# Optimization experiments

Hardware: AMD Instinct MI355X
Metric: run time of the kernel (lower is better)

Reference implementation:

```python
import math
import jax, jax.numpy as jnp
import numpy as np

B, LD, LE = 8, 512, 512
D, H, DK, F, L, V = 1024, 16, 64, 4096, 3, 32000
EPS = 1e-5
NEG = -1000000000.0


def setup_inputs() -> dict:
    key = jax.random.key(0)
    ks = jax.random.split(key, 16)
    s = 0.02
    dec_inputs = jax.random.randint(ks[0], (B, LD), 0, V)
    # causal mask: True = masked out (matches masked_fill semantics)
    self_mask = jnp.broadcast_to(jnp.triu(jnp.ones((LD, LD), bool), k=1), (B, LD, LD))
    enc_output = jax.random.normal(ks[1], (B, LE, D), jnp.float32)
    encoder_mask = jnp.zeros((B, LD, LE), bool)  # no encoder padding
    embed = jax.random.normal(ks[2], (V, D), jnp.float32) * s
    # sinusoidal positional encoding, pe[:LD]
    pos = jnp.arange(LD, dtype=jnp.float32)[:, None]
    div = jnp.exp(jnp.arange(0, D, 2, dtype=jnp.float32) * (-math.log(10000.0) / D))
    pe = jnp.zeros((LD, D), jnp.float32)
    pe = pe.at[:, 0::2].set(jnp.sin(pos * div)).at[:, 1::2].set(jnp.cos(pos * div))
    # per-layer params; axis 1 of attn params: 0=self-attn, 1=enc-dec attn
    wq = jax.random.normal(ks[3], (L, 2, D, D), jnp.float32) * s
    wk = jax.random.normal(ks[4], (L, 2, D, D), jnp.float32) * s
    wv = jax.random.normal(ks[5], (L, 2, D, D), jnp.float32) * s
    wo = jax.random.normal(ks[6], (L, 2, D, D), jnp.float32) * s
    bq = jnp.zeros((L, 2, D), jnp.float32)
    bk = jnp.zeros((L, 2, D), jnp.float32)
    bv = jnp.zeros((L, 2, D), jnp.float32)
    bo = jnp.zeros((L, 2, D), jnp.float32)
    ffn_w1 = jax.random.normal(ks[7], (L, F, D), jnp.float32) * s
    ffn_b1 = jnp.zeros((L, F), jnp.float32)
    ffn_w2 = jax.random.normal(ks[8], (L, D, F), jnp.float32) * s
    ffn_b2 = jnp.zeros((L, D), jnp.float32)
    ln_g = jnp.ones((L, 3, D), jnp.float32)   # norm1/2/3 gains
    ln_b = jnp.zeros((L, 3, D), jnp.float32)  # norm1/2/3 biases
    return dict(dec_inputs=dec_inputs, self_mask=self_mask, enc_output=enc_output,
                encoder_mask=encoder_mask, embed=embed, pe=pe,
                wq=wq, bq=bq, wk=wk, bk=bk, wv=wv, bv=bv, wo=wo, bo=bo,
                ffn_w1=ffn_w1, ffn_b1=ffn_b1, ffn_w2=ffn_w2, ffn_b2=ffn_b2,
                ln_g=ln_g, ln_b=ln_b)


def _ln(x, g, b):
    m = jnp.mean(x, axis=-1, keepdims=True)
    v = jnp.mean((x - m) ** 2, axis=-1, keepdims=True)
    return (x - m) * jax.lax.rsqrt(v + EPS) * g + b


def _mha(qi, ki, vi, mask, wq, bq, wk, bk, wv, bv, wo, bo):
    Bq, Lq, _ = qi.shape
    Lk = ki.shape[1]
    Q = (qi @ wq.T + bq).reshape(Bq, Lq, H, DK).transpose(0, 2, 1, 3)
    K = (ki @ wk.T + bk).reshape(Bq, Lk, H, DK).transpose(0, 2, 1, 3)
    Vv = (vi @ wv.T + bv).reshape(Bq, Lk, H, DK).transpose(0, 2, 1, 3)
    scores = jnp.einsum('bhqd,bhkd->bhqk', Q, K) / math.sqrt(DK)
    scores = jnp.where(mask[:, None, :, :], NEG, scores)
    attn = jax.nn.softmax(scores, axis=-1)
    ctx = jnp.einsum('bhqk,bhkd->bhqd', attn, Vv)
    ctx = ctx.transpose(0, 2, 1, 3).reshape(Bq, Lq, H * DK)
    return ctx @ wo.T + bo


def reference(dec_inputs, self_mask, enc_output, encoder_mask, embed, pe,
              wq, bq, wk, bk, wv, bv, wo, bo,
              ffn_w1, ffn_b1, ffn_w2, ffn_b2, ln_g, ln_b):
    x = embed[dec_inputs] * math.sqrt(D) + pe[None, :, :]
    for l in range(L):
        h = _ln(x, ln_g[l, 0], ln_b[l, 0])
        a = _mha(h, h, h, self_mask,
                 wq[l, 0], bq[l, 0], wk[l, 0], bk[l, 0], wv[l, 0], bv[l, 0], wo[l, 0], bo[l, 0])
        x = x + a
        h = _ln(x, ln_g[l, 1], ln_b[l, 1])
        c = _mha(h, enc_output, enc_output, encoder_mask,
                 wq[l, 1], bq[l, 1], wk[l, 1], bk[l, 1], wv[l, 1], bv[l, 1], wo[l, 1], bo[l, 1])
        x = x + c
        h = _ln(x, ln_g[l, 2], ln_b[l, 2])
        f = jax.nn.relu(h @ ffn_w1[l].T + ffn_b1[l]) @ ffn_w2[l].T + ffn_b2[l]
        # faithful quirk of the source: residual is the cross-attn output, not x
        x = c + f
    return x
```

## Files before the change

### kernel.cpp

```cpp
#include <hip/hip_runtime.h>
#include <hip/hip_bf16.h>

using bf16x8 = __attribute__((ext_vector_type(8))) short;
using f32x4  = __attribute__((ext_vector_type(4))) float;
using u16x4  = __attribute__((ext_vector_type(4))) unsigned short;

#define DEVI static __device__ __forceinline__

DEVI unsigned short f2b(float f) {
  unsigned int u = __float_as_uint(f);
  u += 0x7FFFu + ((u >> 16) & 1u);
  return (unsigned short)(u >> 16);
}

DEVI void gload16(const unsigned short* g, unsigned short* l) {
  __builtin_amdgcn_global_load_lds(
      (const __attribute__((address_space(1))) unsigned int*)g,
      (__attribute__((address_space(3))) unsigned int*)l, 16, 0, 0);
}

DEVI float wred_max16(float v) {
#pragma unroll
  for (int m = 1; m < 16; m <<= 1) v = fmaxf(v, __shfl_xor(v, m, 64));
  return v;
}
DEVI float wred_sum16(float v) {
#pragma unroll
  for (int m = 1; m < 16; m <<= 1) v += __shfl_xor(v, m, 64);
  return v;
}


__global__ void cvt_kernel(const float* __restrict__ in,
                           unsigned short* __restrict__ out, int n4) {
  int i = blockIdx.x * blockDim.x + threadIdx.x;
  const int stride = gridDim.x * blockDim.x;
  for (; i < n4; i += stride) {
    const float4 v = ((const float4*)in)[i];
    u16x4 o;
    o[0] = f2b(v.x); o[1] = f2b(v.y); o[2] = f2b(v.z); o[3] = f2b(v.w);
    ((u16x4*)out)[i] = o;
  }
}

__global__ void pack_w(const float* __restrict__ s0,
                       const float* __restrict__ s1,
                       const float* __restrict__ s2,
                       int sub, unsigned short* __restrict__ dst, int nm) {
  const int r = blockIdx.x;
  const int m = blockIdx.y;
  const int l = blockIdx.z;
  const float* src = (m == 0 ? s0 : m == 1 ? s1 : s2)
                   + (size_t)(l * 2 + sub) * 1048576 + (size_t)r * 1024;
  unsigned short* d = dst + ((size_t)(l * nm + m) * 1024 + r) * 1024;
  const int col = threadIdx.x * 4;
  const float4 v = *(const float4*)(src + col);
  u16x4 o;
  o[0] = f2b(v.x); o[1] = f2b(v.y); o[2] = f2b(v.z); o[3] = f2b(v.w);
  *(u16x4*)(d + col) = o;
}

__global__ void pack_bias(const float* __restrict__ s0,
                          const float* __restrict__ s1,
                          const float* __restrict__ s2,
                          int sub, float* __restrict__ dst, int nm) {
  const int m = blockIdx.x, l = blockIdx.y;
  const float* src = (m == 0 ? s0 : m == 1 ? s1 : s2) + (size_t)(l * 2 + sub) * 1024;
  float* d = dst + ((size_t)l * nm + m) * 1024;
  const int i = threadIdx.x * 4;
  *(float4*)(d + i) = *(const float4*)(src + i);
}

__global__ void embed_kernel(const int* __restrict__ ids,
                             const float* __restrict__ emb,
                             const float* __restrict__ pe,
                             float* __restrict__ x) {
  const int row = blockIdx.x;
  const int t = row & 511;
  const int col = threadIdx.x * 4;
  const int id = ids[row];
  const float4 e = *(const float4*)(emb + (size_t)id * 1024 + col);
  const float4 p = *(const float4*)(pe + (size_t)t * 1024 + col);
  float4 o;
  o.x = e.x * 32.f + p.x; o.y = e.y * 32.f + p.y;
  o.z = e.z * 32.f + p.z; o.w = e.w * 32.f + p.w;
  *(float4*)(x + (size_t)row * 1024 + col) = o;
}

__global__ void ln_kernel(const float* __restrict__ x,
                          const float* __restrict__ g,
                          const float* __restrict__ b,
                          unsigned short* __restrict__ out) {
  const int row = blockIdx.x;
  const int l = threadIdx.x;
  const float4* xr = (const float4*)(x + (size_t)row * 1024);
  float4 v[4];
  float s = 0.f;
#pragma unroll
  for (int i = 0; i < 4; ++i) {
    v[i] = xr[l * 4 + i];
    s += v[i].x + v[i].y + v[i].z + v[i].w;
  }
#pragma unroll
  for (int m = 1; m < 64; m <<= 1) s += __shfl_xor(s, m, 64);
  const float mean = s * (1.f / 1024.f);
  float vs = 0.f;
#pragma unroll
  for (int i = 0; i < 4; ++i) {
    float dx = v[i].x - mean, dy = v[i].y - mean, dz = v[i].z - mean, dw = v[i].w - mean;
    vs += dx * dx + dy * dy + dz * dz + dw * dw;
  }
#pragma unroll
  for (int m = 1; m < 64; m <<= 1) vs += __shfl_xor(vs, m, 64);
  const float inv = rsqrtf(vs * (1.f / 1024.f) + 1e-5f);
#pragma unroll
  for (int i = 0; i < 4; ++i) {
    const int col = l * 16 + i * 4;
    const float4 gg = *(const float4*)(g + col);
    const float4 bb = *(const float4*)(b + col);
    u16x4 o;
    o[0] = f2b((v[i].x - mean) * inv * gg.x + bb.x);
    o[1] = f2b((v[i].y - mean) * inv * gg.y + bb.y);
    o[2] = f2b((v[i].z - mean) * inv * gg.z + bb.z);
    o[3] = f2b((v[i].w - mean) * inv * gg.w + bb.w);
    *(u16x4*)(out + (size_t)row * 1024 + col) = o;
  }
}

__global__ void vt_kernel(const unsigned short* __restrict__ Vsrc, int vsd,
                          unsigned short* __restrict__ Vt) {
  __shared__ alignas(16) unsigned short t[64][72];
  const int tt = blockIdx.x;
  const int h  = blockIdx.y;
  const int b  = blockIdx.z;
  const int tid = threadIdx.x;
  const int r  = tid >> 2;
  const int ch = tid & 3;
  const unsigned short* src =
      Vsrc + (size_t)(b * 512 + tt * 64 + r) * vsd + (size_t)h * 64 + ch * 16;
  const bf16x8 v0 = *(const bf16x8*)src;
  const bf16x8 v1 = *(const bf16x8*)(src + 8);
#pragma unroll
  for (int j = 0; j < 8; ++j) {
    t[ch * 16 + j][r]     = (unsigned short)v0[j];
    t[ch * 16 + 8 + j][r] = (unsigned short)v1[j];
  }
  __syncthreads();
  const int d  = tid >> 2;
  const int tp = tid & 3;
  unsigned short* dst = Vt + (((size_t)(b * 16 + h) * 64 + d) * 512) + tt * 64 + tp * 16;
  *(bf16x8*)dst       = *(const bf16x8*)&t[d][tp * 16];
  *(bf16x8*)(dst + 8) = *(const bf16x8*)&t[d][tp * 16 + 8];
}


enum { EPI_BF16 = 0, EPI_RELU_BF16 = 1, EPI_RES = 2, EPI_RES2 = 3 };

template<int EPI, int BM, int BN>
__global__ void gemm_bt(const unsigned short* __restrict__ A,
                        const unsigned short* __restrict__ Bw,
                        const float* __restrict__ bias,
                        int N, int K, int nn,
                        void* out0, const float* res, float* out1) {
  constexpr int MI = BM / 32;
  constexpr int NJ = BN / 32;
  __shared__ alignas(16) unsigned short As[2][BM * 64];
  __shared__ alignas(16) unsigned short Bs[2][BN * 64];
  const int tid = threadIdx.x;
  const int lane = tid & 63;
  const int wave = tid >> 6;
  int id = blockIdx.x;
  const int nwg = gridDim.x;
  id = (id & 7) * (nwg >> 3) + (id >> 3);
  const int bx = id % nn;
  const int by = id / nn;
  const int m0 = by * BM;
  const int n0 = bx * BN;
  const int wm = (wave >> 1) * (BM / 2);
  const int wn = (wave & 1) * (BN / 2);

  auto stage = [&](int buf, int kt) {
    const size_t k0 = (size_t)kt * 64;
#pragma unroll
    for (int i = 0; i < MI; ++i) {
      const int c = tid + 256 * i;
      const int row = c >> 3;
      const int lc = (c & 7) ^ (row & 7);
      gload16(A + (size_t)(m0 + row) * K + k0 + lc * 8, &As[buf][c * 8]);
    }
#pragma unroll
    for (int i = 0; i < NJ; ++i) {
      const int c = tid + 256 * i;
      const int row = c >> 3;
      const int lc = (c & 7) ^ (row & 7);
      gload16(Bw + (size_t)(n0 + row) * K + k0 + lc * 8, &Bs[buf][c * 8]);
    }
  };

  f32x4 acc[MI][NJ];
#pragma unroll
  for (int i = 0; i < MI; ++i)
#pragma unroll
    for (int j = 0; j < NJ; ++j) acc[i][j] = f32x4{0.f, 0.f, 0.f, 0.f};

  const int nk = K >> 6;
  stage(0, 0);
  int cur = 0;
  const int ro = lane & 15;
  const int hi = lane >> 4;
  for (int kt = 0; kt < nk; ++kt) {
    __syncthreads();
    if (kt + 1 < nk) stage(cur ^ 1, kt + 1);
    bf16x8 af[MI][2], bf[NJ][2];
#pragma unroll
    for (int i = 0; i < MI; ++i) {
      const int r = wm + i * 16 + ro;
#pragma unroll
      for (int ks = 0; ks < 2; ++ks)
        af[i][ks] = *(const bf16x8*)&As[cur][r * 64 + (((ks << 2) + hi) ^ (r & 7)) * 8];
    }
#pragma unroll
    for (int j = 0; j < NJ; ++j) {
      const int r = wn + j * 16 + ro;
#pragma unroll
      for (int ks = 0; ks < 2; ++ks)
        bf[j][ks] = *(const bf16x8*)&Bs[cur][r * 64 + (((ks << 2) + hi) ^ (r & 7)) * 8];
    }
#pragma unroll
    for (int ks = 0; ks < 2; ++ks)
#pragma unroll
      for (int i = 0; i < MI; ++i)
#pragma unroll
        for (int j = 0; j < NJ; ++j)
          acc[i][j] = __builtin_amdgcn_mfma_f32_16x16x32_bf16(af[i][ks], bf[j][ks], acc[i][j], 0, 0, 0);
    cur ^= 1;
  }

  const int r4 = hi * 4;
#pragma unroll
  for (int i = 0; i < MI; ++i) {
#pragma unroll
    for (int j = 0; j < NJ; ++j) {
      const int cg = n0 + wn + j * 16 + ro;
      const float bv = bias[cg];
#pragma unroll
      for (int q = 0; q < 4; ++q) {
        const int rg = m0 + wm + i * 16 + r4 + q;
        const size_t idx = (size_t)rg * N + cg;
        const float v = acc[i][j][q] + bv;
        if (EPI == EPI_BF16) {
          ((unsigned short*)out0)[idx] = f2b(v);
        } else if (EPI == EPI_RELU_BF16) {
          ((unsigned short*)out0)[idx] = f2b(fmaxf(v, 0.f));
        } else if (EPI == EPI_RES) {
          ((float*)out0)[idx] = res[idx] + v;
        } else {
          const float r = res[idx];
          ((float*)out0)[idx] = v;
          out1[idx] = r + v;
        }
      }
    }
  }
}


template<bool CAUSAL>
__global__ __launch_bounds__(64) void attn_kernel(
    const unsigned short* __restrict__ Qg, int qs,
    const unsigned short* __restrict__ Kg, int ksd,
    const unsigned short* __restrict__ Vt,
    unsigned short* __restrict__ Og) {
  __shared__ alignas(16) unsigned short Pl[32 * 64];
  const int qt = blockIdx.x;
  const int h  = blockIdx.y;
  const int b  = blockIdx.z;
  const int lane = threadIdx.x;
  const int ro = lane & 15;
  const int hi = lane >> 4;
  const size_t qbase = (size_t)b * 512 * qs  + (size_t)h * 64;
  const size_t kbase = (size_t)b * 512 * ksd + (size_t)h * 64;
  const size_t vbase = ((size_t)(b * 16 + h)) * 64 * 512;
  const size_t obase = (size_t)b * 512 * 1024 + (size_t)h * 64;

  bf16x8 qf[2][2];
#pragma unroll
  for (int mi = 0; mi < 2; ++mi)
#pragma unroll
    for (int ks = 0; ks < 2; ++ks)
      qf[mi][ks] = *(const bf16x8*)&Qg[qbase + (size_t)(qt * 32 + mi * 16 + ro) * qs + ks * 32 + hi * 8];

  f32x4 o[2][4];
  float mrun[2][4], lrun[2][4];
#pragma unroll
  for (int mi = 0; mi < 2; ++mi) {
#pragma unroll
    for (int di = 0; di < 4; ++di) o[mi][di] = f32x4{0.f, 0.f, 0.f, 0.f};
#pragma unroll
    for (int q = 0; q < 4; ++q) { mrun[mi][q] = -1e30f; lrun[mi][q] = 0.f; }
  }

  const int ktmax = CAUSAL ? (qt >> 1) : 7;
  for (int kt = 0; kt <= ktmax; ++kt) {
    bf16x8 kf[4][2];
#pragma unroll
    for (int ni = 0; ni < 4; ++ni)
#pragma unroll
      for (int ks = 0; ks < 2; ++ks)
        kf[ni][ks] = *(const bf16x8*)&Kg[kbase + (size_t)(kt * 64 + ni * 16 + ro) * ksd + ks * 32 + hi * 8];

    f32x4 s[2][4];
#pragma unroll
    for (int mi = 0; mi < 2; ++mi)
#pragma unroll
      for (int ni = 0; ni < 4; ++ni) s[mi][ni] = f32x4{0.f, 0.f, 0.f, 0.f};
#pragma unroll
    for (int ks = 0; ks < 2; ++ks)
#pragma unroll
      for (int mi = 0; mi < 2; ++mi)
#pragma unroll
        for (int ni = 0; ni < 4; ++ni)
          s[mi][ni] = __builtin_amdgcn_mfma_f32_16x16x32_bf16(qf[mi][ks], kf[ni][ks], s[mi][ni], 0, 0, 0);

#pragma unroll
    for (int mi = 0; mi < 2; ++mi)
#pragma unroll
      for (int ni = 0; ni < 4; ++ni)
#pragma unroll
        for (int q = 0; q < 4; ++q) {
          float e = s[mi][ni][q] * 0.125f;
          if (CAUSAL && kt == ktmax &&
              (kt * 64 + ni * 16 + ro) > (qt * 32 + mi * 16 + hi * 4 + q)) e = -1e9f;
          s[mi][ni][q] = e;
        }

    float fac[2][4];
#pragma unroll
    for (int mi = 0; mi < 2; ++mi)
#pragma unroll
      for (int q = 0; q < 4; ++q) {
        float rm = s[mi][0][q];
#pragma unroll
        for (int ni = 1; ni < 4; ++ni) rm = fmaxf(rm, s[mi][ni][q]);
        rm = wred_max16(rm);
        const float mn = fmaxf(mrun[mi][q], rm);
        fac[mi][q] = __expf(mrun[mi][q] - mn);
        mrun[mi][q] = mn;
      }
#pragma unroll
    for (int mi = 0; mi < 2; ++mi)
#pragma unroll
      for (int q = 0; q < 4; ++q) {
        float rs = 0.f;
#pragma unroll
        for (int ni = 0; ni < 4; ++ni) {
          const float pv = __expf(s[mi][ni][q] - mrun[mi][q]);
          s[mi][ni][q] = pv;
          rs += pv;
        }
        rs = wred_sum16(rs);
        lrun[mi][q] = lrun[mi][q] * fac[mi][q] + rs;
      }
#pragma unroll
    for (int mi = 0; mi < 2; ++mi)
#pragma unroll
      for (int di = 0; di < 4; ++di)
#pragma unroll
        for (int q = 0; q < 4; ++q) o[mi][di][q] *= fac[mi][q];

#pragma unroll
    for (int mi = 0; mi < 2; ++mi)
#pragma unroll
      for (int ni = 0; ni < 4; ++ni)
#pragma unroll
        for (int q = 0; q < 4; ++q) {
          const int row = mi * 16 + hi * 4 + q;
          const int col = ni * 16 + ro;
          const int sc  = ((col >> 3) ^ (row & 7)) * 8 + (col & 7);
          Pl[row * 64 + sc] = f2b(s[mi][ni][q]);
        }

    bf16x8 pa[2][2];
#pragma unroll
    for (int mi = 0; mi < 2; ++mi)
#pragma unroll
      for (int ks = 0; ks < 2; ++ks) {
        const int row = mi * 16 + ro;
        pa[mi][ks] = *(const bf16x8*)&Pl[row * 64 + (((ks << 2) + hi) ^ (row & 7)) * 8];
      }

#pragma unroll
    for (int di = 0; di < 4; ++di)
#pragma unroll
      for (int ks = 0; ks < 2; ++ks) {
        const bf16x8 vf = *(const bf16x8*)&Vt[vbase + (size_t)(di * 16 + ro) * 512 + kt * 64 + ks * 32 + hi * 8];
#pragma unroll
        for (int mi = 0; mi < 2; ++mi)
          o[mi][di] = __builtin_amdgcn_mfma_f32_16x16x32_bf16(pa[mi][ks], vf, o[mi][di], 0, 0, 0);
      }
  }

#pragma unroll
  for (int mi = 0; mi < 2; ++mi)
#pragma unroll
    for (int di = 0; di < 4; ++di)
#pragma unroll
      for (int q = 0; q < 4; ++q) {
        const float val = o[mi][di][q] / lrun[mi][q];
        Og[obase + (size_t)(qt * 32 + mi * 16 + hi * 4 + q) * 1024 + di * 16 + ro] = f2b(val);
      }
}


extern "C" void kernel_launch(void* const* d_in, const int* in_sizes, int n_in,
                              void* d_out, int out_size, void* d_ws, size_t ws_size,
                              hipStream_t stream) {
  (void)in_sizes; (void)n_in; (void)out_size; (void)ws_size;
  const int*   dec = (const int*)d_in[0];
  const float* enc = (const float*)d_in[2];
  const float* emb = (const float*)d_in[4];
  const float* pe  = (const float*)d_in[5];
  const float* wq  = (const float*)d_in[6];
  const float* bq  = (const float*)d_in[7];
  const float* wk  = (const float*)d_in[8];
  const float* bk  = (const float*)d_in[9];
  const float* wv  = (const float*)d_in[10];
  const float* bv  = (const float*)d_in[11];
  const float* wo  = (const float*)d_in[12];
  const float* bo  = (const float*)d_in[13];
  const float* w1  = (const float*)d_in[14];
  const float* b1  = (const float*)d_in[15];
  const float* w2  = (const float*)d_in[16];
  const float* b2  = (const float*)d_in[17];
  const float* lng = (const float*)d_in[18];
  const float* lnb = (const float*)d_in[19];

  const size_t SZ_ACT = 4194304ull;

  char* p = (char*)d_ws;
  auto alloc = [&](size_t bytes) { char* r = p; p += (bytes + 255) & ~(size_t)255; return r; };
  unsigned short* qkvw  = (unsigned short*)alloc(3ull * 3 * 1048576 * 2);
  unsigned short* kvw   = (unsigned short*)alloc(3ull * 2 * 1048576 * 2);
  unsigned short* wqxb  = (unsigned short*)alloc(3ull * 1048576 * 2);
  unsigned short* Wob   = (unsigned short*)alloc(6291456ull * 2);
  unsigned short* W1b   = (unsigned short*)alloc(12582912ull * 2);
  unsigned short* W2b   = (unsigned short*)alloc(12582912ull * 2);
  unsigned short* encb  = (unsigned short*)alloc(SZ_ACT * 2);
  float*          x     = (float*)alloc(SZ_ACT * 4);
  float*          c     = (float*)alloc(SZ_ACT * 4);
  unsigned short* hb    = (unsigned short*)alloc(SZ_ACT * 2);
  unsigned short* qkvb  = (unsigned short*)alloc(4096ull * 3072 * 2);
  unsigned short* kvb   = (unsigned short*)alloc(4096ull * 2048 * 2);
  unsigned short* qb    = (unsigned short*)alloc(SZ_ACT * 2);
  unsigned short* vtb   = (unsigned short*)alloc(SZ_ACT * 2);
  unsigned short* mid   = (unsigned short*)alloc(4096ull * 4096 * 2);
  float*          qkvbias = (float*)alloc(3ull * 3072 * 4);
  float*          kvbias  = (float*)alloc(3ull * 2048 * 4);

  cvt_kernel<<<2048, 256, 0, stream>>>(wo, Wob, 1572864);
  cvt_kernel<<<2048, 256, 0, stream>>>(w1, W1b, 3145728);
  cvt_kernel<<<2048, 256, 0, stream>>>(w2, W2b, 3145728);
  cvt_kernel<<<2048, 256, 0, stream>>>(enc, encb, 1048576);
  pack_w<<<dim3(1024, 3, 3), 256, 0, stream>>>(wq, wk, wv, 0, qkvw, 3);
  pack_w<<<dim3(1024, 2, 3), 256, 0, stream>>>(wk, wv, wv, 1, kvw, 2);
  pack_w<<<dim3(1024, 1, 3), 256, 0, stream>>>(wq, wq, wq, 1, wqxb, 1);
  pack_bias<<<dim3(3, 3), 256, 0, stream>>>(bq, bk, bv, 0, qkvbias, 3);
  pack_bias<<<dim3(2, 3), 256, 0, stream>>>(bk, bv, bv, 1, kvbias, 2);
  embed_kernel<<<4096, 256, 0, stream>>>(dec, emb, pe, x);

  const dim3 gAttn(16, 16, 8);
  const dim3 gVt(8, 16, 8);

  for (int l = 0; l < 3; ++l) {
    const float* g0 = lng + (l * 3 + 0) * 1024; const float* e0 = lnb + (l * 3 + 0) * 1024;
    const float* g1 = lng + (l * 3 + 1) * 1024; const float* e1 = lnb + (l * 3 + 1) * 1024;
    const float* g2 = lng + (l * 3 + 2) * 1024; const float* e2 = lnb + (l * 3 + 2) * 1024;

    ln_kernel<<<4096, 64, 0, stream>>>(x, g0, e0, hb);
    gemm_bt<EPI_BF16, 128, 128><<<32 * 24, 256, 0, stream>>>(hb, qkvw + (size_t)l * 3 * 1048576,
        qkvbias + l * 3072, 3072, 1024, 24, qkvb, nullptr, nullptr);
    vt_kernel<<<gVt, 256, 0, stream>>>(qkvb + 2048, 3072, vtb);
    attn_kernel<true><<<gAttn, 64, 0, stream>>>(qkvb, 3072, qkvb + 1024, 3072, vtb, hb);
    gemm_bt<EPI_RES, 128, 64><<<32 * 16, 256, 0, stream>>>(hb, Wob + (size_t)(l * 2) * 1048576,
        bo + (l * 2) * 1024, 1024, 1024, 16, x, x, nullptr);

    ln_kernel<<<4096, 64, 0, stream>>>(x, g1, e1, hb);
    gemm_bt<EPI_BF16, 128, 64><<<32 * 16, 256, 0, stream>>>(hb, wqxb + (size_t)l * 1048576,
        bq + (l * 2 + 1) * 1024, 1024, 1024, 16, qb, nullptr, nullptr);
    gemm_bt<EPI_BF16, 128, 128><<<32 * 16, 256, 0, stream>>>(encb, kvw + (size_t)l * 2 * 1048576,
        kvbias + l * 2048, 2048, 1024, 16, kvb, nullptr, nullptr);
    vt_kernel<<<gVt, 256, 0, stream>>>(kvb + 1024, 2048, vtb);
    attn_kernel<false><<<gAttn, 64, 0, stream>>>(qb, 1024, kvb, 2048, vtb, hb);
    gemm_bt<EPI_RES2, 128, 64><<<32 * 16, 256, 0, stream>>>(hb, Wob + (size_t)(l * 2 + 1) * 1048576,
        bo + (l * 2 + 1) * 1024, 1024, 1024, 16, c, x, x);

    ln_kernel<<<4096, 64, 0, stream>>>(x, g2, e2, hb);
    gemm_bt<EPI_RELU_BF16, 128, 128><<<32 * 32, 256, 0, stream>>>(hb, W1b + (size_t)l * 4194304,
        b1 + l * 4096, 4096, 1024, 32, mid, nullptr, nullptr);
    float* xout = (l == 2) ? (float*)d_out : x;
    gemm_bt<EPI_RES, 128, 64><<<32 * 16, 256, 0, stream>>>(mid, W2b + (size_t)l * 4194304,
        b2 + l * 1024, 1024, 4096, 16, xout, c, nullptr);
  }
}
```

Measured before the change: 1.177 ms.

## Add 256x128 triple-buffered GEMM and batch encoder K/V projections across layers

Introduces a new 512-thread GEMM kernel with 256x128 tiles, a three-stage LDS pipeline using direct global-to-LDS loads and XOR swizzle, and uses it for the QKV and FFN1 projections. The encoder K/V projections for all three layers are hoisted into a single N=6144 GEMM before the layer loop, because enc_output does not change between layers. Attention and vt kernels then read per-layer slices with stride 6144. The costs are a larger kvb workspace, higher LDS use per block (about 144 KB), and coarser tiles that give fewer blocks for the N=3072 GEMM.

```diff
diff --git a/kernel.cpp b/kernel.cpp
--- a/kernel.cpp
+++ b/kernel.cpp
@@ -151,6 +151,122 @@
   unsigned short* dst = Vt + (((size_t)(b * 16 + h) * 64 + d) * 512) + tt * 64 + tp * 16;
   *(bf16x8*)dst       = *(const bf16x8*)&t[d][tp * 16];
   *(bf16x8*)(dst + 8) = *(const bf16x8*)&t[d][tp * 16 + 8];
+}
+
+
+template<int EPI>
+__global__ __launch_bounds__(512, 2) void gemm256(
+    const unsigned short* __restrict__ A,
+    const unsigned short* __restrict__ Bw,
+    const float* __restrict__ bias,
+    int N, unsigned short* __restrict__ out0) {
+  constexpr int K = 1024, NK = 16;
+  __shared__ alignas(16) unsigned short As0[256 * 64];
+  __shared__ alignas(16) unsigned short As1[256 * 64];
+  __shared__ alignas(16) unsigned short As2[256 * 64];
+  __shared__ alignas(16) unsigned short Bs0[128 * 64];
+  __shared__ alignas(16) unsigned short Bs1[128 * 64];
+  __shared__ alignas(16) unsigned short Bs2[128 * 64];
+  const int tid = threadIdx.x;
+  const int lane = tid & 63;
+  const int wave = tid >> 6;
+  const int wr = wave >> 2;
+  const int wc = wave & 3;
+  int id = blockIdx.x;
+  const int nwg = gridDim.x;
+  id = (id & 7) * (nwg >> 3) + (id >> 3);
+  const int nn = N >> 7;
+  const int bx = id % nn;
+  const int by = id / nn;
+  const int m0 = by * 256;
+  const int n0 = bx * 128;
+  const int ro = lane & 15;
+  const int hi = lane >> 4;
+
+  auto stageA = [&](unsigned short* dst, int kt) {
+    const size_t k0 = (size_t)kt * 64;
+#pragma unroll
+    for (int i = 0; i < 4; ++i) {
+      const int c = tid + 512 * i;
+      const int row = c >> 3;
+      const int lc = (c & 7) ^ (row & 7);
+      gload16(A + (size_t)(m0 + row) * K + k0 + lc * 8, dst + c * 8);
+    }
+  };
+  auto stageB = [&](unsigned short* dst, int kt) {
+    const size_t k0 = (size_t)kt * 64;
+#pragma unroll
+    for (int i = 0; i < 2; ++i) {
+      const int c = tid + 512 * i;
+      const int row = c >> 3;
+      const int lc = (c & 7) ^ (row & 7);
+      gload16(Bw + (size_t)(n0 + row) * K + k0 + lc * 8, dst + c * 8);
+    }
+  };
+
+  f32x4 acc[8][2];
+#pragma unroll
+  for (int i = 0; i < 8; ++i)
+#pragma unroll
+    for (int j = 0; j < 2; ++j) acc[i][j] = f32x4{0.f, 0.f, 0.f, 0.f};
+
+  stageA(As0, 0); stageB(Bs0, 0);
+  stageA(As1, 1); stageB(Bs1, 1);
+
+  auto body = [&](int kt, const unsigned short* Ac, const unsigned short* Bc,
+                  unsigned short* An, unsigned short* Bn, bool last) {
+    if (last) asm volatile("s_waitcnt vmcnt(0)" ::: "memory");
+    else      asm volatile("s_waitcnt vmcnt(6)" ::: "memory");
+    __builtin_amdgcn_s_barrier();
+    if (kt + 2 < NK) { stageA(An, kt + 2); stageB(Bn, kt + 2); }
+    bf16x8 af[8][2], bf[2][2];
+#pragma unroll
+    for (int mi = 0; mi < 8; ++mi) {
+      const int r = wr * 128 + mi * 16 + ro;
+#pragma unroll
+      for (int ks = 0; ks < 2; ++ks)
+        af[mi][ks] = *(const bf16x8*)&Ac[r * 64 + (((ks << 2) + hi) ^ (r & 7)) * 8];
+    }
+#pragma unroll
+    for (int nj = 0; nj < 2; ++nj) {
+      const int r = wc * 32 + nj * 16 + ro;
+#pragma unroll
+      for (int ks = 0; ks < 2; ++ks)
+        bf[nj][ks] = *(const bf16x8*)&Bc[r * 64 + (((ks << 2) + hi) ^ (r & 7)) * 8];
+    }
+    __builtin_amdgcn_s_setprio(1);
+#pragma unroll
+    for (int ks = 0; ks < 2; ++ks)
+#pragma unroll
+      for (int mi = 0; mi < 8; ++mi)
+#pragma unroll
+        for (int nj = 0; nj < 2; ++nj)
+          acc[mi][nj] = __builtin_amdgcn_mfma_f32_16x16x32_bf16(af[mi][ks], bf[nj][ks], acc[mi][nj], 0, 0, 0);
+    __builtin_amdgcn_s_setprio(0);
+  };
+
+  for (int base = 0; base < 15; base += 3) {
+    body(base,     As0, Bs0, As2, Bs2, false);
+    body(base + 1, As1, Bs1, As0, Bs0, false);
+    body(base + 2, As2, Bs2, As1, Bs1, false);
+  }
+  body(15, As0, Bs0, As1, Bs1, true);
+
+  const int r4 = hi * 4;
+#pragma unroll
+  for (int mi = 0; mi < 8; ++mi) {
+#pragma unroll
+    for (int nj = 0; nj < 2; ++nj) {
+      const int cg = n0 + wc * 32 + nj * 16 + ro;
+      const float bv = bias[cg];
+#pragma unroll
+      for (int q = 0; q < 4; ++q) {
+        const int rg = m0 + wr * 128 + mi * 16 + r4 + q;
+        const float v = acc[mi][nj][q] + bv;
+        out0[(size_t)rg * N + cg] = f2b(EPI == 1 ? fmaxf(v, 0.f) : v);
+      }
+    }
+  }
 }
 
 
@@ -450,7 +566,7 @@
   float*          c     = (float*)alloc(SZ_ACT * 4);
   unsigned short* hb    = (unsigned short*)alloc(SZ_ACT * 2);
   unsigned short* qkvb  = (unsigned short*)alloc(4096ull * 3072 * 2);
-  unsigned short* kvb   = (unsigned short*)alloc(4096ull * 2048 * 2);
+  unsigned short* kvb   = (unsigned short*)alloc(4096ull * 6144 * 2);
   unsigned short* qb    = (unsigned short*)alloc(SZ_ACT * 2);
   unsigned short* vtb   = (unsigned short*)alloc(SZ_ACT * 2);
   unsigned short* mid   = (unsigned short*)alloc(4096ull * 4096 * 2);
@@ -468,6 +584,8 @@
   pack_bias<<<dim3(2, 3), 256, 0, stream>>>(bk, bv, bv, 1, kvbias, 2);
   embed_kernel<<<4096, 256, 0, stream>>>(dec, emb, pe, x);
 
+  gemm256<0><<<48 * 16, 512, 0, stream>>>(encb, kvw, kvbias, 6144, kvb);
+
   const dim3 gAttn(16, 16, 8);
   const dim3 gVt(8, 16, 8);
 
@@ -477,8 +595,8 @@
     const float* g2 = lng + (l * 3 + 2) * 1024; const float* e2 = lnb + (l * 3 + 2) * 1024;
 
     ln_kernel<<<4096, 64, 0, stream>>>(x, g0, e0, hb);
-    gemm_bt<EPI_BF16, 128, 128><<<32 * 24, 256, 0, stream>>>(hb, qkvw + (size_t)l * 3 * 1048576,
-        qkvbias + l * 3072, 3072, 1024, 24, qkvb, nullptr, nullptr);
+    gemm256<0><<<24 * 16, 512, 0, stream>>>(hb, qkvw + (size_t)l * 3 * 1048576,
+        qkvbias + l * 3072, 3072, qkvb);
     vt_kernel<<<gVt, 256, 0, stream>>>(qkvb + 2048, 3072, vtb);
     attn_kernel<true><<<gAttn, 64, 0, stream>>>(qkvb, 3072, qkvb + 1024, 3072, vtb, hb);
     gemm_bt<EPI_RES, 128, 64><<<32 * 16, 256, 0, stream>>>(hb, Wob + (size_t)(l * 2) * 1048576,
@@ -487,16 +605,14 @@
     ln_kernel<<<4096, 64, 0, stream>>>(x, g1, e1, hb);
     gemm_bt<EPI_BF16, 128, 64><<<32 * 16, 256, 0, stream>>>(hb, wqxb + (size_t)l * 1048576,
         bq + (l * 2 + 1) * 1024, 1024, 1024, 16, qb, nullptr, nullptr);
-    gemm_bt<EPI_BF16, 128, 128><<<32 * 16, 256, 0, stream>>>(encb, kvw + (size_t)l * 2 * 1048576,
-        kvbias + l * 2048, 2048, 1024, 16, kvb, nullptr, nullptr);
-    vt_kernel<<<gVt, 256, 0, stream>>>(kvb + 1024, 2048, vtb);
-    attn_kernel<false><<<gAttn, 64, 0, stream>>>(qb, 1024, kvb, 2048, vtb, hb);
+    vt_kernel<<<gVt, 256, 0, stream>>>(kvb + l * 2048 + 1024, 6144, vtb);
+    attn_kernel<false><<<gAttn, 64, 0, stream>>>(qb, 1024, kvb + l * 2048, 6144, vtb, hb);
     gemm_bt<EPI_RES2, 128, 64><<<32 * 16, 256, 0, stream>>>(hb, Wob + (size_t)(l * 2 + 1) * 1048576,
         bo + (l * 2 + 1) * 1024, 1024, 1024, 16, c, x, x);
 
     ln_kernel<<<4096, 64, 0, stream>>>(x, g2, e2, hb);
-    gemm_bt<EPI_RELU_BF16, 128, 128><<<32 * 32, 256, 0, stream>>>(hb, W1b + (size_t)l * 4194304,
-        b1 + l * 4096, 4096, 1024, 32, mid, nullptr, nullptr);
+    gemm256<1><<<32 * 16, 512, 0, stream>>>(hb, W1b + (size_t)l * 4194304,
+        b1 + l * 4096, 4096, mid);
     float* xout = (l == 2) ? (float*)d_out : x;
     gemm_bt<EPI_RES, 128, 64><<<32 * 16, 256, 0, stream>>>(mid, W2b + (size_t)l * 4194304,
         b2 + l * 1024, 1024, 4096, 16, xout, c, nullptr);
```

New measurement: 1.183 ms. No clear change (+0.5%).
